# Kernel tuning notes

Hardware: AMD Instinct MI355X
Metric: run time of the kernel (lower is better)

## Reference

```python
import jax, jax.numpy as jnp
import numpy as np

D_IN = 1024
D_OUT = 1024
SEQ = 2048
BATCH = 4


def setup_inputs() -> dict:
    key = jax.random.key(0)
    ks = jax.random.split(key, 7)
    s_in = 1.0 / np.sqrt(D_IN)
    return {
        "x": jax.random.normal(ks[0], (BATCH, SEQ, D_IN), dtype=jnp.float32),
        "Wq": jax.random.normal(ks[1], (D_IN, D_OUT), dtype=jnp.float32) * s_in,
        "bq": jax.random.normal(ks[2], (D_OUT,), dtype=jnp.float32) * 0.01,
        "Wk": jax.random.normal(ks[3], (D_IN, D_OUT), dtype=jnp.float32) * s_in,
        "bk": jax.random.normal(ks[4], (D_OUT,), dtype=jnp.float32) * 0.01,
        "Wv": jax.random.normal(ks[5], (D_IN, D_OUT), dtype=jnp.float32) * s_in,
        "bv": jax.random.normal(ks[6], (D_OUT,), dtype=jnp.float32) * 0.01,
    }


def reference(x, Wq, bq, Wk, bk, Wv, bv):
    # x: [b, n, d_in]
    b, n, d_in = x.shape
    q = x @ Wq + bq  # [b, n, d_out]
    k = x @ Wk + bk
    v = x @ Wv + bv
    scale = 1.0 / jnp.sqrt(jnp.asarray(d_in, x.dtype))
    scores = jnp.einsum("bqd,bkd->bqk", q, k) * scale  # [b, n, n]
    causal = jnp.triu(jnp.ones((n, n), dtype=bool), k=1)  # True above diagonal
    scores = jnp.where(causal, -jnp.inf, scores)
    weights = jax.nn.softmax(scores, axis=-1)
    # dropout p=0.0 -> identity
    context = jnp.einsum("bqk,bkd->bqd", weights, v)
    return context
```

## Files before the change

kernel.cpp:

```cpp
#include <hip/hip_runtime.h>

typedef unsigned short u16;
typedef __bf16 bf16x8 __attribute__((ext_vector_type(8)));
typedef float floatx4 __attribute__((ext_vector_type(4)));

#define B_ 4
#define SEQ 2048
#define DIM 1024

__device__ __forceinline__ u16 f2bf(float f) {
    unsigned u = __builtin_bit_cast(unsigned, f);
    u += 0x7FFFu + ((u >> 16) & 1u);
    return (u16)(u >> 16);
}
__device__ __forceinline__ float bf2f(u16 h) {
    unsigned u = ((unsigned)h) << 16;
    return __builtin_bit_cast(float, u);
}

#define GPTR(p) ((const __attribute__((address_space(1))) void*)(p))
#define LPTR(p) ((__attribute__((address_space(3))) void*)(p))

__global__ __launch_bounds__(256) void convert_x(const float4* __restrict__ x,
                                                 ushort4* __restrict__ xb) {
    int i = blockIdx.x * 256 + threadIdx.x;
    float4 v = x[i];
    ushort4 o;
    o.x = f2bf(v.x); o.y = f2bf(v.y); o.z = f2bf(v.z); o.w = f2bf(v.w);
    xb[i] = o;
}

__global__ __launch_bounds__(256) void transpose_w(const float* __restrict__ Wq,
                                                   const float* __restrict__ Wk,
                                                   const float* __restrict__ Wv,
                                                   u16* __restrict__ Wt) {
    __shared__ u16 t[64][66];
    const int z = blockIdx.z;
    const float* W = (z == 0) ? Wq : ((z == 1) ? Wk : Wv);
    u16* out = Wt + (size_t)z * DIM * DIM;
    const int tx = threadIdx.x, ty = threadIdx.y;
    const int k0 = blockIdx.x * 64, n0 = blockIdx.y * 64;
#pragma unroll
    for (int j = 0; j < 8; j++) {
        int k = ty + 8 * j;
        float2 v = *(const float2*)(W + (size_t)(k0 + k) * DIM + n0 + 2 * tx);
        t[2 * tx][k] = f2bf(v.x);
        t[2 * tx + 1][k] = f2bf(v.y);
    }
    __syncthreads();
#pragma unroll
    for (int j = 0; j < 8; j++) {
        int n = ty + 8 * j;
        ushort2 o;
        o.x = t[n][2 * tx];
        o.y = t[n][2 * tx + 1];
        *(ushort2*)(out + (size_t)(n0 + n) * DIM + k0 + 2 * tx) = o;
    }
}

__device__ __forceinline__ void mainloop(
    const u16* __restrict__ Ab, const u16* __restrict__ Bb, int lda, int ldb,
    int Kt, u16* lsA, u16* lsB, int tid, int wave, int quad, int l15,
    int wm, int wn, floatx4 (&acc)[4][4]) {
    const int srow = tid >> 2;
    const int scol = ((tid & 3) ^ ((tid >> 3) & 3)) * 8;
    const u16* gA = Ab + (size_t)srow * lda + scol;
    const u16* gB = Bb + (size_t)srow * ldb + scol;
    const int swq = (quad ^ ((l15 >> 1) & 3)) * 8;

#pragma unroll
    for (int i = 0; i < 4; i++)
#pragma unroll
        for (int j = 0; j < 4; j++) {
            floatx4 zz = {0.f, 0.f, 0.f, 0.f};
            acc[i][j] = zz;
        }

    for (int k0 = 0; k0 < Kt; k0 += 64) {
#pragma unroll
        for (int h = 0; h < 2; h++)
#pragma unroll
            for (int c = 0; c < 2; c++) {
                __builtin_amdgcn_global_load_lds(
                    GPTR(gA + (size_t)c * 64 * lda + h * 32),
                    LPTR(lsA + h * 4096 + c * 2048 + wave * 512), 16, 0, 0);
                __builtin_amdgcn_global_load_lds(
                    GPTR(gB + (size_t)c * 64 * ldb + h * 32),
                    LPTR(lsB + h * 4096 + c * 2048 + wave * 512), 16, 0, 0);
            }
        gA += 64; gB += 64;
        __syncthreads();

#pragma unroll
        for (int h = 0; h < 2; h++) {
            bf16x8 af[4];
#pragma unroll
            for (int i = 0; i < 4; i++)
                af[i] = *(const bf16x8*)(lsA + h * 4096 + (wm + i * 16 + l15) * 32 + swq);
#pragma unroll
            for (int j = 0; j < 4; j++) {
                bf16x8 bfr = *(const bf16x8*)(lsB + h * 4096 + (wn + j * 16 + l15) * 32 + swq);
#pragma unroll
                for (int i = 0; i < 4; i++)
                    acc[i][j] = __builtin_amdgcn_mfma_f32_16x16x32_bf16(af[i], bfr, acc[i][j], 0, 0, 0);
            }
        }
        __syncthreads();
    }
}

__global__ __launch_bounds__(256, 3) void gemm_qkv(
    const u16* __restrict__ A, const u16* __restrict__ Bt, u16* __restrict__ QK,
    const float* __restrict__ b0, const float* __restrict__ b1, const float* __restrict__ b2,
    u16* __restrict__ VtOut) {
    __shared__ union {
        struct { u16 a[128 * 64]; u16 b[128 * 64]; } stage;
        u16 epT[64 * 136];
    } sm;
    const int tid = threadIdx.x;
    const int wave = tid >> 6, lane = tid & 63;
    const int quad = lane >> 4, l15 = lane & 15;
    const int wm = (wave >> 1) * 64, wn = (wave & 1) * 64;
    const int z = blockIdx.x >> 3, xn = blockIdx.x & 7, yb = blockIdx.y;

    const u16* Ab = A + (size_t)yb * 128 * DIM;
    const u16* Bb = Bt + (size_t)z * DIM * DIM + (size_t)xn * 128 * DIM;
    floatx4 acc[4][4];
    mainloop(Ab, Bb, DIM, DIM, DIM, sm.stage.a, sm.stage.b,
             tid, wave, quad, l15, wm, wn, acc);

    const int colbase = xn * 128;
    const int mq = quad * 4;
    const float* bias = (z == 0) ? b0 : ((z == 1) ? b1 : b2);
    const int n0 = colbase + wn + l15;

    if (z < 2) {
        u16* Cb = QK + (size_t)z * B_ * SEQ * DIM;
        const int m0 = yb * 128 + wm + mq;
#pragma unroll
        for (int j = 0; j < 4; j++) {
            float bv_ = bias[n0 + j * 16];
#pragma unroll
            for (int i = 0; i < 4; i++)
#pragma unroll
                for (int r = 0; r < 4; r++)
                    Cb[(size_t)(m0 + i * 16 + r) * DIM + (n0 + j * 16)] = f2bf(acc[i][j][r] + bv_);
        }
        return;
    }

    float addj[4];
#pragma unroll
    for (int j = 0; j < 4; j++) addj[j] = bias[n0 + j * 16];
    const int b = (yb * 128) >> 11;
    const int sb = (yb * 128) & (SEQ - 1);
    u16* Vb = VtOut + (size_t)b * DIM * SEQ;
#pragma unroll
    for (int c = 0; c < 2; c++) {
        __syncthreads();
        if ((wave & 1) == c) {
#pragma unroll
            for (int i = 0; i < 4; i++)
#pragma unroll
                for (int j = 0; j < 4; j++)
#pragma unroll
                    for (int r = 0; r < 4; r++) {
                        int lr = wm + i * 16 + mq + r;
                        int lc = j * 16 + l15;
                        sm.epT[lc * 136 + lr] = f2bf(acc[i][j][r] + addj[j]);
                    }
        }
        __syncthreads();
#pragma unroll
        for (int k = 0; k < 4; k++) {
            int s2 = tid + 256 * k;
            int n = s2 >> 4, seg = s2 & 15;
            uint4 val = *(const uint4*)&sm.epT[n * 136 + seg * 8];
            *(uint4*)(Vb + (size_t)(colbase + c * 64 + n) * SEQ + sb + seg * 8) = val;
        }
    }
}

__global__ __launch_bounds__(256, 3) void gemm_scores(
    const u16* __restrict__ Q, const u16* __restrict__ K, u16* __restrict__ S,
    float scale) {
    const int ym = gridDim.y - 1 - blockIdx.y;
    if ((int)blockIdx.x > ym) return;

    __shared__ u16 lsA[128 * 64];
    __shared__ u16 lsB[128 * 64];
    const int tid = threadIdx.x;
    const int wave = tid >> 6, lane = tid & 63;
    const int quad = lane >> 4, l15 = lane & 15;
    const int wm = (wave >> 1) * 64, wn = (wave & 1) * 64;
    const int z = blockIdx.z;

    const u16* Ab = Q + (size_t)z * SEQ * DIM + (size_t)ym * 128 * DIM;
    const u16* Bb = K + (size_t)z * SEQ * DIM + (size_t)blockIdx.x * 128 * DIM;
    floatx4 acc[4][4];
    mainloop(Ab, Bb, DIM, DIM, DIM, lsA, lsB,
             tid, wave, quad, l15, wm, wn, acc);

    u16* Cb = S + (size_t)z * SEQ * SEQ;
    const int m0 = ym * 128 + wm + quad * 4;
    const int n0 = blockIdx.x * 128 + wn + l15;
#pragma unroll
    for (int j = 0; j < 4; j++)
#pragma unroll
        for (int i = 0; i < 4; i++)
#pragma unroll
            for (int r = 0; r < 4; r++)
                Cb[(size_t)(m0 + i * 16 + r) * SEQ + (n0 + j * 16)] = f2bf(acc[i][j][r] * scale);
}

__global__ __launch_bounds__(256, 3) void gemm_pv(
    const u16* __restrict__ P, const u16* __restrict__ Vt, float* __restrict__ O) {
    const int ym = gridDim.y - 1 - blockIdx.y;
    __shared__ u16 lsA[128 * 64];
    __shared__ u16 lsB[128 * 64];
    const int tid = threadIdx.x;
    const int wave = tid >> 6, lane = tid & 63;
    const int quad = lane >> 4, l15 = lane & 15;
    const int wm = (wave >> 1) * 64, wn = (wave & 1) * 64;
    const int z = blockIdx.z;

    const u16* Ab = P + (size_t)z * SEQ * SEQ + (size_t)ym * 128 * SEQ;
    const u16* Bb = Vt + (size_t)z * DIM * SEQ + (size_t)blockIdx.x * 128 * SEQ;
    const int Kt = (ym + 1) * 128;
    floatx4 acc[4][4];
    mainloop(Ab, Bb, SEQ, SEQ, Kt, lsA, lsB,
             tid, wave, quad, l15, wm, wn, acc);

    float* Cf = O + (size_t)z * SEQ * DIM;
    const int m0 = ym * 128 + wm + quad * 4;
    const int n0 = blockIdx.x * 128 + wn + l15;
#pragma unroll
    for (int j = 0; j < 4; j++)
#pragma unroll
        for (int i = 0; i < 4; i++)
#pragma unroll
            for (int r = 0; r < 4; r++)
                Cf[(size_t)(m0 + i * 16 + r) * DIM + (n0 + j * 16)] = acc[i][j][r];
}

__global__ __launch_bounds__(256) void softmax_causal(u16* __restrict__ S) {
    const int q = blockIdx.x, b = blockIdx.y, tid = threadIdx.x;
    u16* row = S + ((size_t)b * SEQ + q) * SEQ;
    const int L = q + 1;
    const int Z = ((q >> 7) + 1) << 7;
    const int k0 = tid * 8;
    __shared__ float redm[4], reds[4];

    uint4 rv = ((const uint4*)row)[tid];
    unsigned w[4] = {rv.x, rv.y, rv.z, rv.w};
    float f[8];
#pragma unroll
    for (int e = 0; e < 8; e++) {
        u16 h = (u16)((w[e >> 1] >> ((e & 1) * 16)) & 0xFFFFu);
        f[e] = (k0 + e < L) ? bf2f(h) : -3.0e38f;
    }
    float m = f[0];
#pragma unroll
    for (int e = 1; e < 8; e++) m = fmaxf(m, f[e]);
#pragma unroll
    for (int o = 32; o > 0; o >>= 1) m = fmaxf(m, __shfl_xor(m, o));
    if ((tid & 63) == 0) redm[tid >> 6] = m;
    __syncthreads();
    m = fmaxf(fmaxf(redm[0], redm[1]), fmaxf(redm[2], redm[3]));

    float p[8];
    float s = 0.f;
#pragma unroll
    for (int e = 0; e < 8; e++) {
        p[e] = (k0 + e < L) ? __expf(f[e] - m) : 0.f;
        s += p[e];
    }
#pragma unroll
    for (int o = 32; o > 0; o >>= 1) s += __shfl_xor(s, o);
    if ((tid & 63) == 0) reds[tid >> 6] = s;
    __syncthreads();
    s = reds[0] + reds[1] + reds[2] + reds[3];
    const float inv = 1.0f / s;

    if (k0 < Z) {
        unsigned o2[4];
#pragma unroll
        for (int e = 0; e < 4; e++) {
            unsigned lo = f2bf(p[2 * e] * inv);
            unsigned hi = f2bf(p[2 * e + 1] * inv);
            o2[e] = lo | (hi << 16);
        }
        uint4 ov = {o2[0], o2[1], o2[2], o2[3]};
        ((uint4*)row)[tid] = ov;
    }
}

extern "C" void kernel_launch(void* const* d_in, const int* in_sizes, int n_in,
                              void* d_out, int out_size, void* d_ws, size_t ws_size,
                              hipStream_t stream) {
    const float* x = (const float*)d_in[0];
    const float* Wq = (const float*)d_in[1];
    const float* bq = (const float*)d_in[2];
    const float* Wk = (const float*)d_in[3];
    const float* bk = (const float*)d_in[4];
    const float* Wv = (const float*)d_in[5];
    const float* bv = (const float*)d_in[6];
    float* out = (float*)d_out;

    char* ws = (char*)d_ws;
    const size_t MB = 1024ull * 1024ull;
    u16* S = (u16*)ws;
    u16* xb = (u16*)ws;
    u16* Wt = (u16*)(ws + 16 * MB);
    u16* QK = (u16*)(ws + 32 * MB);
    u16* Vt = (u16*)(ws + 64 * MB);
    const size_t MAT = (size_t)B_ * SEQ * DIM;
    u16* Q = QK;
    u16* Km = QK + MAT;

    const float scale = 0.03125f;

    convert_x<<<8192, 256, 0, stream>>>((const float4*)x, (ushort4*)xb);
    transpose_w<<<dim3(16, 16, 3), dim3(32, 8), 0, stream>>>(Wq, Wk, Wv, Wt);
    gemm_qkv<<<dim3(24, 64), 256, 0, stream>>>(xb, Wt, QK, bq, bk, bv, Vt);
    gemm_scores<<<dim3(16, 16, 4), 256, 0, stream>>>(Q, Km, S, scale);
    softmax_causal<<<dim3(SEQ, B_), 256, 0, stream>>>(S);
    gemm_pv<<<dim3(8, 16, 4), 256, 0, stream>>>(S, Vt, out);
}
```

Before: 249.6 us.

## Double-buffer LDS tiles in scores and PV GEMMs to overlap loads with MFMA

```diff
diff --git a/kernel.cpp b/kernel.cpp
--- a/kernel.cpp
+++ b/kernel.cpp
@@ -58,6 +58,41 @@
     }
 }
 
+__device__ __forceinline__ void issue_loads(const u16* gA, const u16* gB,
+                                            int lda, int ldb,
+                                            u16* lsA, u16* lsB, int wave) {
+#pragma unroll
+    for (int h = 0; h < 2; h++)
+#pragma unroll
+        for (int c = 0; c < 2; c++) {
+            __builtin_amdgcn_global_load_lds(
+                GPTR(gA + (size_t)c * 64 * lda + h * 32),
+                LPTR(lsA + h * 4096 + c * 2048 + wave * 512), 16, 0, 0);
+            __builtin_amdgcn_global_load_lds(
+                GPTR(gB + (size_t)c * 64 * ldb + h * 32),
+                LPTR(lsB + h * 4096 + c * 2048 + wave * 512), 16, 0, 0);
+        }
+}
+
+__device__ __forceinline__ void compute_tile(const u16* lsA, const u16* lsB,
+                                             int wm, int wn, int l15, int swq,
+                                             floatx4 (&acc)[4][4]) {
+#pragma unroll
+    for (int h = 0; h < 2; h++) {
+        bf16x8 af[4];
+#pragma unroll
+        for (int i = 0; i < 4; i++)
+            af[i] = *(const bf16x8*)(lsA + h * 4096 + (wm + i * 16 + l15) * 32 + swq);
+#pragma unroll
+        for (int j = 0; j < 4; j++) {
+            bf16x8 bfr = *(const bf16x8*)(lsB + h * 4096 + (wn + j * 16 + l15) * 32 + swq);
+#pragma unroll
+            for (int i = 0; i < 4; i++)
+                acc[i][j] = __builtin_amdgcn_mfma_f32_16x16x32_bf16(af[i], bfr, acc[i][j], 0, 0, 0);
+        }
+    }
+}
+
 __device__ __forceinline__ void mainloop(
     const u16* __restrict__ Ab, const u16* __restrict__ Bb, int lda, int ldb,
     int Kt, u16* lsA, u16* lsB, int tid, int wave, int quad, int l15,
@@ -77,35 +112,46 @@
         }
 
     for (int k0 = 0; k0 < Kt; k0 += 64) {
-#pragma unroll
-        for (int h = 0; h < 2; h++)
-#pragma unroll
-            for (int c = 0; c < 2; c++) {
-                __builtin_amdgcn_global_load_lds(
-                    GPTR(gA + (size_t)c * 64 * lda + h * 32),
-                    LPTR(lsA + h * 4096 + c * 2048 + wave * 512), 16, 0, 0);
-                __builtin_amdgcn_global_load_lds(
-                    GPTR(gB + (size_t)c * 64 * ldb + h * 32),
-                    LPTR(lsB + h * 4096 + c * 2048 + wave * 512), 16, 0, 0);
-            }
+        issue_loads(gA, gB, lda, ldb, lsA, lsB, wave);
         gA += 64; gB += 64;
         __syncthreads();
-
-#pragma unroll
-        for (int h = 0; h < 2; h++) {
-            bf16x8 af[4];
-#pragma unroll
-            for (int i = 0; i < 4; i++)
-                af[i] = *(const bf16x8*)(lsA + h * 4096 + (wm + i * 16 + l15) * 32 + swq);
-#pragma unroll
-            for (int j = 0; j < 4; j++) {
-                bf16x8 bfr = *(const bf16x8*)(lsB + h * 4096 + (wn + j * 16 + l15) * 32 + swq);
-#pragma unroll
-                for (int i = 0; i < 4; i++)
-                    acc[i][j] = __builtin_amdgcn_mfma_f32_16x16x32_bf16(af[i], bfr, acc[i][j], 0, 0, 0);
-            }
-        }
+        compute_tile(lsA, lsB, wm, wn, l15, swq, acc);
         __syncthreads();
+    }
+}
+
+__device__ __forceinline__ void mainloop_db(
+    const u16* __restrict__ Ab, const u16* __restrict__ Bb, int lda, int ldb,
+    int Kt, u16* lsA, u16* lsB, int tid, int wave, int quad, int l15,
+    int wm, int wn, floatx4 (&acc)[4][4]) {
+    const int srow = tid >> 2;
+    const int scol = ((tid & 3) ^ ((tid >> 3) & 3)) * 8;
+    const u16* gA = Ab + (size_t)srow * lda + scol;
+    const u16* gB = Bb + (size_t)srow * ldb + scol;
+    const int swq = (quad ^ ((l15 >> 1) & 3)) * 8;
+
+#pragma unroll
+    for (int i = 0; i < 4; i++)
+#pragma unroll
+        for (int j = 0; j < 4; j++) {
+            floatx4 zz = {0.f, 0.f, 0.f, 0.f};
+            acc[i][j] = zz;
+        }
+
+    issue_loads(gA, gB, lda, ldb, lsA, lsB, wave);
+    for (int k0 = 0; k0 < Kt; k0 += 64) {
+        const int cur = (k0 >> 6) & 1;
+        gA += 64; gB += 64;
+        if (k0 + 64 < Kt) {
+            issue_loads(gA, gB, lda, ldb,
+                        lsA + (cur ^ 1) * 8192, lsB + (cur ^ 1) * 8192, wave);
+            __builtin_amdgcn_s_waitcnt(0xF78);
+        } else {
+            __builtin_amdgcn_s_waitcnt(0xF70);
+        }
+        __builtin_amdgcn_s_barrier();
+        compute_tile(lsA + cur * 8192, lsB + cur * 8192, wm, wn, l15, swq, acc);
+        __builtin_amdgcn_s_barrier();
     }
 }
 
@@ -181,14 +227,14 @@
     }
 }
 
-__global__ __launch_bounds__(256, 3) void gemm_scores(
+__global__ __launch_bounds__(256, 2) void gemm_scores(
     const u16* __restrict__ Q, const u16* __restrict__ K, u16* __restrict__ S,
     float scale) {
     const int ym = gridDim.y - 1 - blockIdx.y;
     if ((int)blockIdx.x > ym) return;
 
-    __shared__ u16 lsA[128 * 64];
-    __shared__ u16 lsB[128 * 64];
+    __shared__ u16 lsA[2][128 * 64];
+    __shared__ u16 lsB[2][128 * 64];
     const int tid = threadIdx.x;
     const int wave = tid >> 6, lane = tid & 63;
     const int quad = lane >> 4, l15 = lane & 15;
@@ -198,8 +244,8 @@
     const u16* Ab = Q + (size_t)z * SEQ * DIM + (size_t)ym * 128 * DIM;
     const u16* Bb = K + (size_t)z * SEQ * DIM + (size_t)blockIdx.x * 128 * DIM;
     floatx4 acc[4][4];
-    mainloop(Ab, Bb, DIM, DIM, DIM, lsA, lsB,
-             tid, wave, quad, l15, wm, wn, acc);
+    mainloop_db(Ab, Bb, DIM, DIM, DIM, lsA[0], lsB[0],
+                tid, wave, quad, l15, wm, wn, acc);
 
     u16* Cb = S + (size_t)z * SEQ * SEQ;
     const int m0 = ym * 128 + wm + quad * 4;
@@ -213,11 +259,11 @@
                 Cb[(size_t)(m0 + i * 16 + r) * SEQ + (n0 + j * 16)] = f2bf(acc[i][j][r] * scale);
 }
 
-__global__ __launch_bounds__(256, 3) void gemm_pv(
+__global__ __launch_bounds__(256, 2) void gemm_pv(
     const u16* __restrict__ P, const u16* __restrict__ Vt, float* __restrict__ O) {
     const int ym = gridDim.y - 1 - blockIdx.y;
-    __shared__ u16 lsA[128 * 64];
-    __shared__ u16 lsB[128 * 64];
+    __shared__ u16 lsA[2][128 * 64];
+    __shared__ u16 lsB[2][128 * 64];
     const int tid = threadIdx.x;
     const int wave = tid >> 6, lane = tid & 63;
     const int quad = lane >> 4, l15 = lane & 15;
@@ -228,8 +274,8 @@
     const u16* Bb = Vt + (size_t)z * DIM * SEQ + (size_t)blockIdx.x * 128 * SEQ;
     const int Kt = (ym + 1) * 128;
     floatx4 acc[4][4];
-    mainloop(Ab, Bb, SEQ, SEQ, Kt, lsA, lsB,
-             tid, wave, quad, l15, wm, wn, acc);
+    mainloop_db(Ab, Bb, SEQ, SEQ, Kt, lsA[0], lsB[0],
+                tid, wave, quad, l15, wm, wn, acc);
 
     float* Cf = O + (size_t)z * SEQ * DIM;
     const int m0 = ym * 128 + wm + quad * 4;
```

Result: no change. 250.2 us (+0.2%).
